# Performance work log

Measured on AMD Instinct MI355X. Metric: run time of the kernel, lower is better.

The kernel has to match this reference:

```python
import jax, jax.numpy as jnp
import numpy as np

EPS = 1e-12   # F.normalize eps
COS_EPS = 1e-8  # F.cosine_similarity eps

B, S, V, D, P, L = 4, 2048, 64, 1024, 8, 24
H = D // 24            # prefix_transform bottleneck = 42
K = 2 * L * D          # 49152 output feature dim


def setup_inputs() -> dict:
    key = jax.random.key(0)
    ks = jax.random.split(key, 8)
    return {
        "prefix": jax.random.randint(ks[0], (B, V), 0, V),
        "ctx_embeds": jax.random.normal(ks[1], (B, S, D), jnp.float32),
        "tables": jax.random.normal(ks[2], (P, V, D), jnp.float32) * 0.02,
        "lora_prefix_emb": jax.random.normal(ks[3], (P, D), jnp.float32),
        "w1": jax.random.normal(ks[4], (D, H), jnp.float32) * 0.02,
        "b1": jnp.zeros((H,), jnp.float32),
        "w2": jax.random.normal(ks[5], (H, K), jnp.float32) * 0.02,
        "b2": jnp.zeros((K,), jnp.float32),
    }


def _gates(ctx_embeds, lora_prefix_emb):
    """select_prefix, vectorized over the num_prefix_set loop.

    The original builds sim_i = bmm(norm(emb), norm(e_i.repeat(B,S,1), dim=0).permute)
    of shape [B,S,S]; since the key is repeated, every column of sim is identical,
    so we carry the column vector [P,B,S] and the math is exact.
    """
    b, s, _ = ctx_embeds.shape
    # normalize embedding over feature dim (F.normalize p=2 dim=2)
    emb_n = ctx_embeds / jnp.maximum(
        jnp.linalg.norm(ctx_embeds, axis=2, keepdims=True), EPS)
    # F.normalize over dim=0 of a tensor repeated B times -> sign(x)/sqrt(B)
    u = lora_prefix_emb / jnp.maximum(
        jnp.sqrt(float(b)) * jnp.abs(lora_prefix_emb), EPS)  # [P,D]
    v = jnp.einsum('bsd,pd->pbs', emb_n, u)          # column of sim matrix
    c = jnp.maximum(v, 0.0)                          # clamp(min=0)
    # F.normalize over last dim (length S, all entries equal c) -> c/(sqrt(S)*c)
    n = c / jnp.maximum(jnp.sqrt(float(s)) * c, EPS)
    w = jax.nn.softmax(n, axis=2)                    # softmax over token dim (dim=1 in torch layout)
    a_v = jnp.einsum('pbs,bsd->pbd', w, ctx_embeds)  # attended value per expert
    e_norm = jnp.linalg.norm(lora_prefix_emb, axis=1)          # [P]
    a_norm = jnp.linalg.norm(a_v, axis=2)                      # [P,B]
    cos = jnp.einsum('pd,pbd->pb', lora_prefix_emb, a_v) / \
        jnp.maximum(e_norm[:, None] * a_norm, COS_EPS)
    return jax.nn.softmax(cos.T, axis=-1)            # self.s_t, [B,P]


def reference(prefix, ctx_embeds, tables, lora_prefix_emb, w1, b1, w2, b2):
    s_t = _gates(ctx_embeds, lora_prefix_emb)        # [B,P]
    # forward() re-applies softmax to self.s_t (faithful double softmax)
    gate = jax.nn.softmax(s_t, axis=-1)              # [B,P]
    tok = tables[:, prefix]                          # [P,B,V,D] per-expert embedding lookup
    h = jnp.tanh(jnp.einsum('pbvd,dh->pbvh', tok, w1) + b1)
    pkv = jnp.einsum('pbvh,hk->pbvk', h, w2) + b2    # [P,B,V,K]
    out = jnp.einsum('bp,pbvk->bvk', gate, pkv)      # gated mixture over experts
    return out
```

## Files before the change

kernel.cpp:

```cpp
#include <hip/hip_runtime.h>

#define BB 4
#define SS 2048
#define VV 64
#define DD 1024
#define PP 8
#define HH 42
#define KK 49152

static constexpr float F_EPS = 1e-12f;
static constexpr float SQRT_S = 45.254833995939045f;

__global__ __launch_bounds__(256) void k1_rowdots(
    const float* __restrict__ ctx, const float* __restrict__ lora,
    float* __restrict__ n_ws) {
  __shared__ float u_lds[PP * DD];
  const int t = threadIdx.x;
  for (int i = t; i < PP * DD; i += 256) {
    float e = lora[i];
    u_lds[i] = e / fmaxf(2.0f * fabsf(e), F_EPS);
  }
  __syncthreads();
  const int wave = t >> 6, lane = t & 63;
  const float4* ctx4 = (const float4*)ctx;
  const float4* u4 = (const float4*)u_lds;
  #pragma unroll
  for (int i = 0; i < 4; ++i) {
    const int r = blockIdx.x * 16 + wave * 4 + i;
    float sumsq = 0.0f;
    float dot[PP];
    #pragma unroll
    for (int p = 0; p < PP; ++p) dot[p] = 0.0f;
    #pragma unroll
    for (int j = 0; j < 4; ++j) {
      float4 c = ctx4[(size_t)r * 256 + j * 64 + lane];
      sumsq += c.x * c.x + c.y * c.y + c.z * c.z + c.w * c.w;
      #pragma unroll
      for (int p = 0; p < PP; ++p) {
        float4 u = u4[p * 256 + j * 64 + lane];
        dot[p] += c.x * u.x + c.y * u.y + c.z * u.z + c.w * u.w;
      }
    }
    #pragma unroll
    for (int m = 32; m >= 1; m >>= 1) {
      sumsq += __shfl_xor(sumsq, m, 64);
      #pragma unroll
      for (int p = 0; p < PP; ++p) dot[p] += __shfl_xor(dot[p], m, 64);
    }
    if (lane == 0) {
      float inv = 1.0f / fmaxf(sqrtf(sumsq), F_EPS);
      float nn[PP];
      #pragma unroll
      for (int p = 0; p < PP; ++p) {
        float v = dot[p] * inv;
        float c = fmaxf(v, 0.0f);
        nn[p] = c / fmaxf(SQRT_S * c, F_EPS);
      }
      float4* o = (float4*)(n_ws + (size_t)r * 8);
      o[0] = make_float4(nn[0], nn[1], nn[2], nn[3]);
      o[1] = make_float4(nn[4], nn[5], nn[6], nn[7]);
    }
  }
}

__global__ __launch_bounds__(256) void k3_av(
    const float* __restrict__ ctx, const float* __restrict__ n_ws,
    float* __restrict__ part) {
  const int t = threadIdx.x;
  const int chunk = blockIdx.x;
  const int b = blockIdx.y;
  const int dz = blockIdx.z;
  __shared__ float zpart[4][PP];
  __shared__ float Zl[PP];
  __shared__ float w_lds[64 * PP];
  float z[PP];
  #pragma unroll
  for (int p = 0; p < PP; ++p) z[p] = 0.0f;
  const float4* n4 = (const float4*)n_ws;
  for (int it = 0; it < 8; ++it) {
    int s = it * 256 + t;
    float4 a = n4[(size_t)(b * SS + s) * 2];
    float4 c = n4[(size_t)(b * SS + s) * 2 + 1];
    z[0] += expf(a.x); z[1] += expf(a.y); z[2] += expf(a.z); z[3] += expf(a.w);
    z[4] += expf(c.x); z[5] += expf(c.y); z[6] += expf(c.z); z[7] += expf(c.w);
  }
  #pragma unroll
  for (int m = 32; m >= 1; m >>= 1) {
    #pragma unroll
    for (int p = 0; p < PP; ++p) z[p] += __shfl_xor(z[p], m, 64);
  }
  const int wave = t >> 6, lane = t & 63;
  if (lane == 0) {
    #pragma unroll
    for (int p = 0; p < PP; ++p) zpart[wave][p] = z[p];
  }
  __syncthreads();
  if (t < PP) Zl[t] = zpart[0][t] + zpart[1][t] + zpart[2][t] + zpart[3][t];
  __syncthreads();
  if (t < 64) {
    int s = chunk * 64 + t;
    #pragma unroll
    for (int p = 0; p < PP; ++p)
      w_lds[t * PP + p] = expf(n_ws[(size_t)(b * SS + s) * 8 + p]) / Zl[p];
  }
  __syncthreads();
  float2 acc[PP];
  #pragma unroll
  for (int p = 0; p < PP; ++p) acc[p] = make_float2(0.f, 0.f);
  const float2* ctx2 = (const float2*)ctx;
  const float4* w4 = (const float4*)w_lds;
  #pragma unroll 4
  for (int sl = 0; sl < 64; ++sl) {
    int s = chunk * 64 + sl;
    float2 c = ctx2[(size_t)(b * SS + s) * 512 + dz * 256 + t];
    float4 wa = w4[sl * 2];
    float4 wb = w4[sl * 2 + 1];
    float w[PP] = {wa.x, wa.y, wa.z, wa.w, wb.x, wb.y, wb.z, wb.w};
    #pragma unroll
    for (int p = 0; p < PP; ++p) {
      acc[p].x += w[p] * c.x;
      acc[p].y += w[p] * c.y;
    }
  }
  float2* part2 = (float2*)part;
  #pragma unroll
  for (int p = 0; p < PP; ++p)
    part2[(size_t)((b * 32 + chunk) * PP + p) * 512 + dz * 256 + t] = acc[p];
}

__global__ __launch_bounds__(256) void k4_cos(
    const float* __restrict__ part, const float* __restrict__ lora,
    float* __restrict__ cos_ws) {
  const int t = threadIdx.x;
  const int p = blockIdx.x, b = blockIdx.y;
  const float4* part4 = (const float4*)part;
  float4 av = make_float4(0.f, 0.f, 0.f, 0.f);
  for (int c = 0; c < 32; ++c) {
    float4 x = part4[(size_t)((b * 32 + c) * PP + p) * 256 + t];
    av.x += x.x; av.y += x.y; av.z += x.z; av.w += x.w;
  }
  float4 e = ((const float4*)lora)[p * 256 + t];
  float dt = av.x * e.x + av.y * e.y + av.z * e.z + av.w * e.w;
  float a2 = av.x * av.x + av.y * av.y + av.z * av.z + av.w * av.w;
  float e2 = e.x * e.x + e.y * e.y + e.z * e.z + e.w * e.w;
  #pragma unroll
  for (int m = 32; m >= 1; m >>= 1) {
    dt += __shfl_xor(dt, m, 64);
    a2 += __shfl_xor(a2, m, 64);
    e2 += __shfl_xor(e2, m, 64);
  }
  __shared__ float red[4][3];
  const int wave = t >> 6, lane = t & 63;
  if (lane == 0) { red[wave][0] = dt; red[wave][1] = a2; red[wave][2] = e2; }
  __syncthreads();
  if (t == 0) {
    float Dv = red[0][0] + red[1][0] + red[2][0] + red[3][0];
    float Av = red[0][1] + red[1][1] + red[2][1] + red[3][1];
    float Ev = red[0][2] + red[1][2] + red[2][2] + red[3][2];
    cos_ws[b * PP + p] = Dv / fmaxf(sqrtf(Ev) * sqrtf(Av), 1e-8f);
  }
}

__global__ __launch_bounds__(256) void k5_hall(
    const float* __restrict__ tables, const float* __restrict__ w1,
    const float* __restrict__ b1, float* __restrict__ h_all) {
  __shared__ float row_lds[DD];
  __shared__ float partial[4 * 64];
  const int t = threadIdx.x;
  const int r = blockIdx.x;
  ((float4*)row_lds)[t] = ((const float4*)(tables + (size_t)r * DD))[t];
  __syncthreads();
  const int h = t & 63, q = t >> 6;
  float acc = 0.0f;
  if (h < HH) {
    const int d0 = q * 256;
    #pragma unroll 8
    for (int dl = 0; dl < 256; ++dl) {
      acc += row_lds[d0 + dl] * w1[(size_t)(d0 + dl) * HH + h];
    }
  }
  partial[q * 64 + h] = acc;
  __syncthreads();
  if (t < HH) {
    float s = partial[t] + partial[64 + t] + partial[128 + t] + partial[192 + t];
    h_all[(size_t)r * HH + t] = tanhf(s + b1[t]);
  }
}

__global__ __launch_bounds__(256) void k7_out(
    const float* __restrict__ w2, const float* __restrict__ b2,
    const float* __restrict__ h_all, const float* __restrict__ cos_ws,
    const int* __restrict__ prefix, float* __restrict__ out) {
  __shared__ float gate_lds[PP];
  __shared__ float hg_lds[HH * 64];
  __shared__ float w2_lds[HH * 128];
  const int t = threadIdx.x;
  const int b = blockIdx.y;
  const size_t kbase = (size_t)blockIdx.x * 128;
  for (int i = t; i < HH * 128; i += 256) {
    int h = i >> 7, kk = i & 127;
    w2_lds[i] = w2[(size_t)h * KK + kbase + kk];
  }
  if (t == 0) {
    float c[PP];
    float m = -1e30f;
    #pragma unroll
    for (int p = 0; p < PP; ++p) { c[p] = cos_ws[b * PP + p]; m = fmaxf(m, c[p]); }
    float s = 0.0f;
    #pragma unroll
    for (int p = 0; p < PP; ++p) { c[p] = expf(c[p] - m); s += c[p]; }
    float inv = 1.0f / s;
    float m2 = -1e30f;
    #pragma unroll
    for (int p = 0; p < PP; ++p) { c[p] *= inv; m2 = fmaxf(m2, c[p]); }
    float s2 = 0.0f;
    #pragma unroll
    for (int p = 0; p < PP; ++p) { c[p] = expf(c[p] - m2); s2 += c[p]; }
    float inv2 = 1.0f / s2;
    #pragma unroll
    for (int p = 0; p < PP; ++p) gate_lds[p] = c[p] * inv2;
  }
  __syncthreads();
  for (int idx = t; idx < 64 * HH; idx += 256) {
    int v = idx / HH;
    int h = idx - v * HH;
    int tokv = prefix[b * VV + v];
    float s = 0.0f;
    #pragma unroll
    for (int p = 0; p < PP; ++p)
      s += gate_lds[p] * h_all[(size_t)(p * VV + tokv) * HH + h];
    hg_lds[h * 64 + v] = s;
  }
  __syncthreads();
  const int tk = t & 31, tb = t >> 5;
  float4 acc[8];
  #pragma unroll
  for (int i = 0; i < 8; ++i) acc[i] = make_float4(0.f, 0.f, 0.f, 0.f);
  const float4* w24 = (const float4*)w2_lds;
  const float4* hg4 = (const float4*)hg_lds;
  #pragma unroll 2
  for (int h = 0; h < HH; ++h) {
    float4 wv = w24[h * 32 + tk];
    float4 g0 = hg4[h * 16 + tb * 2];
    float4 g1 = hg4[h * 16 + tb * 2 + 1];
    float gg[8] = {g0.x, g0.y, g0.z, g0.w, g1.x, g1.y, g1.z, g1.w};
    #pragma unroll
    for (int i = 0; i < 8; ++i) {
      acc[i].x += gg[i] * wv.x;
      acc[i].y += gg[i] * wv.y;
      acc[i].z += gg[i] * wv.z;
      acc[i].w += gg[i] * wv.w;
    }
  }
  float4 b2v = ((const float4*)b2)[(kbase >> 2) + tk];
  float4* out4 = (float4*)out;
  #pragma unroll
  for (int i = 0; i < 8; ++i) {
    int bv = b * 64 + tb * 8 + i;
    float4 o;
    o.x = acc[i].x + b2v.x;
    o.y = acc[i].y + b2v.y;
    o.z = acc[i].z + b2v.z;
    o.w = acc[i].w + b2v.w;
    out4[(((size_t)bv * KK + kbase) >> 2) + tk] = o;
  }
}

extern "C" void kernel_launch(void* const* d_in, const int* in_sizes, int n_in,
                              void* d_out, int out_size, void* d_ws, size_t ws_size,
                              hipStream_t stream) {
  const int* prefix = (const int*)d_in[0];
  const float* ctx = (const float*)d_in[1];
  const float* tables = (const float*)d_in[2];
  const float* lora = (const float*)d_in[3];
  const float* w1 = (const float*)d_in[4];
  const float* b1 = (const float*)d_in[5];
  const float* w2 = (const float*)d_in[6];
  const float* b2 = (const float*)d_in[7];
  float* out = (float*)d_out;
  char* ws = (char*)d_ws;
  float* n_ws = (float*)ws;
  float* part = (float*)(ws + 262144);
  float* cos_ws = (float*)(ws + 262144 + 4194304);
  float* h_all = (float*)(ws + 262144 + 4194304 + 128);

  k1_rowdots<<<512, 256, 0, stream>>>(ctx, lora, n_ws);
  k5_hall<<<512, 256, 0, stream>>>(tables, w1, b1, h_all);
  k3_av<<<dim3(32, 4, 2), 256, 0, stream>>>(ctx, n_ws, part);
  k4_cos<<<dim3(8, 4), 256, 0, stream>>>(part, lora, cos_ws);
  k7_out<<<dim3(384, 4), 256, 0, stream>>>(w2, b2, h_all, cos_ws, prefix, out);
}
```

Before: 170.0 us.

## Fuse row-dot and hidden-projection kernels into one launch with batched rows

Merges the ctx row-dot gating kernel and the tables×w1 hidden projection into one 1024-block launch, with block index choosing the branch, so the two independent stages run concurrently and one launch is saved. The row-dot branch now loads four rows at once to reuse each LDS u vector and raise memory-level parallelism. It also replaces the per-expert full butterfly with a partial reduce plus a select-and-transpose shuffle, so eight lanes write results. The fused kernel allocates 32KB of LDS for every block, including the small hidden-projection blocks, which may reduce their occupancy. A partial-sum loop in k4_cos also gets an unroll pragma.

```diff
diff --git a/kernel.cpp b/kernel.cpp
--- a/kernel.cpp
+++ b/kernel.cpp
@@ -11,54 +11,95 @@
 static constexpr float F_EPS = 1e-12f;
 static constexpr float SQRT_S = 45.254833995939045f;
 
-__global__ __launch_bounds__(256) void k1_rowdots(
+__global__ __launch_bounds__(256) void k15_fused(
     const float* __restrict__ ctx, const float* __restrict__ lora,
-    float* __restrict__ n_ws) {
-  __shared__ float u_lds[PP * DD];
+    const float* __restrict__ tables, const float* __restrict__ w1,
+    const float* __restrict__ b1, float* __restrict__ n_ws,
+    float* __restrict__ h_all) {
+  __shared__ float smem[PP * DD];
   const int t = threadIdx.x;
-  for (int i = t; i < PP * DD; i += 256) {
-    float e = lora[i];
-    u_lds[i] = e / fmaxf(2.0f * fabsf(e), F_EPS);
-  }
-  __syncthreads();
-  const int wave = t >> 6, lane = t & 63;
-  const float4* ctx4 = (const float4*)ctx;
-  const float4* u4 = (const float4*)u_lds;
-  #pragma unroll
-  for (int i = 0; i < 4; ++i) {
-    const int r = blockIdx.x * 16 + wave * 4 + i;
-    float sumsq = 0.0f;
-    float dot[PP];
-    #pragma unroll
-    for (int p = 0; p < PP; ++p) dot[p] = 0.0f;
+  if (blockIdx.x < 512) {
+    for (int i = t; i < PP * DD; i += 256) {
+      float e = lora[i];
+      smem[i] = e / fmaxf(2.0f * fabsf(e), F_EPS);
+    }
+    __syncthreads();
+    const int wave = t >> 6, lane = t & 63;
+    const int rbase = blockIdx.x * 16 + wave * 4;
+    const float4* ctx4 = (const float4*)ctx;
+    const float4* u4 = (const float4*)smem;
+    float dot[4][PP];
+    float sq[4] = {0.f, 0.f, 0.f, 0.f};
+    #pragma unroll
+    for (int i = 0; i < 4; ++i)
+      #pragma unroll
+      for (int p = 0; p < PP; ++p) dot[i][p] = 0.f;
     #pragma unroll
     for (int j = 0; j < 4; ++j) {
-      float4 c = ctx4[(size_t)r * 256 + j * 64 + lane];
-      sumsq += c.x * c.x + c.y * c.y + c.z * c.z + c.w * c.w;
+      float4 c[4];
+      #pragma unroll
+      for (int i = 0; i < 4; ++i)
+        c[i] = ctx4[(size_t)(rbase + i) * 256 + j * 64 + lane];
+      #pragma unroll
+      for (int i = 0; i < 4; ++i)
+        sq[i] += c[i].x * c[i].x + c[i].y * c[i].y + c[i].z * c[i].z + c[i].w * c[i].w;
       #pragma unroll
       for (int p = 0; p < PP; ++p) {
         float4 u = u4[p * 256 + j * 64 + lane];
-        dot[p] += c.x * u.x + c.y * u.y + c.z * u.z + c.w * u.w;
+        #pragma unroll
+        for (int i = 0; i < 4; ++i)
+          dot[i][p] += c[i].x * u.x + c[i].y * u.y + c[i].z * u.z + c[i].w * u.w;
       }
     }
-    #pragma unroll
-    for (int m = 32; m >= 1; m >>= 1) {
-      sumsq += __shfl_xor(sumsq, m, 64);
-      #pragma unroll
-      for (int p = 0; p < PP; ++p) dot[p] += __shfl_xor(dot[p], m, 64);
-    }
-    if (lane == 0) {
-      float inv = 1.0f / fmaxf(sqrtf(sumsq), F_EPS);
-      float nn[PP];
-      #pragma unroll
-      for (int p = 0; p < PP; ++p) {
-        float v = dot[p] * inv;
-        float c = fmaxf(v, 0.0f);
-        nn[p] = c / fmaxf(SQRT_S * c, F_EPS);
+    const int sel = lane & 7;
+    #pragma unroll
+    for (int i = 0; i < 4; ++i) {
+      float s = sq[i];
+      #pragma unroll
+      for (int m = 32; m >= 1; m >>= 1) s += __shfl_xor(s, m, 64);
+      float d0 = dot[i][0], d1 = dot[i][1], d2 = dot[i][2], d3 = dot[i][3];
+      float d4 = dot[i][4], d5 = dot[i][5], d6 = dot[i][6], d7 = dot[i][7];
+      #pragma unroll
+      for (int m = 1; m <= 4; m <<= 1) {
+        d0 += __shfl_xor(d0, m, 64); d1 += __shfl_xor(d1, m, 64);
+        d2 += __shfl_xor(d2, m, 64); d3 += __shfl_xor(d3, m, 64);
+        d4 += __shfl_xor(d4, m, 64); d5 += __shfl_xor(d5, m, 64);
+        d6 += __shfl_xor(d6, m, 64); d7 += __shfl_xor(d7, m, 64);
       }
-      float4* o = (float4*)(n_ws + (size_t)r * 8);
-      o[0] = make_float4(nn[0], nn[1], nn[2], nn[3]);
-      o[1] = make_float4(nn[4], nn[5], nn[6], nn[7]);
+      float v = d0;
+      v = (sel == 1) ? d1 : v; v = (sel == 2) ? d2 : v;
+      v = (sel == 3) ? d3 : v; v = (sel == 4) ? d4 : v;
+      v = (sel == 5) ? d5 : v; v = (sel == 6) ? d6 : v;
+      v = (sel == 7) ? d7 : v;
+      v += __shfl_xor(v, 8, 64);
+      v += __shfl_xor(v, 16, 64);
+      v += __shfl_xor(v, 32, 64);
+      if (lane < PP) {
+        float inv = 1.0f / fmaxf(sqrtf(s), F_EPS);
+        float c = fmaxf(v * inv, 0.0f);
+        n_ws[(size_t)(rbase + i) * 8 + lane] = c / fmaxf(SQRT_S * c, F_EPS);
+      }
+    }
+  } else {
+    float* row_lds = smem;
+    float* partial = smem + DD;
+    const int r = blockIdx.x - 512;
+    ((float4*)row_lds)[t] = ((const float4*)(tables + (size_t)r * DD))[t];
+    __syncthreads();
+    const int h = t & 63, q = t >> 6;
+    float acc = 0.0f;
+    if (h < HH) {
+      const int d0 = q * 256;
+      #pragma unroll 8
+      for (int dl = 0; dl < 256; ++dl) {
+        acc += row_lds[d0 + dl] * w1[(size_t)(d0 + dl) * HH + h];
+      }
+    }
+    partial[q * 64 + h] = acc;
+    __syncthreads();
+    if (t < HH) {
+      float s = partial[t] + partial[64 + t] + partial[128 + t] + partial[192 + t];
+      h_all[(size_t)r * HH + t] = tanhf(s + b1[t]);
     }
   }
 }
@@ -135,6 +176,7 @@
   const int p = blockIdx.x, b = blockIdx.y;
   const float4* part4 = (const float4*)part;
   float4 av = make_float4(0.f, 0.f, 0.f, 0.f);
+  #pragma unroll 8
   for (int c = 0; c < 32; ++c) {
     float4 x = part4[(size_t)((b * 32 + c) * PP + p) * 256 + t];
     av.x += x.x; av.y += x.y; av.z += x.z; av.w += x.w;
@@ -158,32 +200,6 @@
     float Av = red[0][1] + red[1][1] + red[2][1] + red[3][1];
     float Ev = red[0][2] + red[1][2] + red[2][2] + red[3][2];
     cos_ws[b * PP + p] = Dv / fmaxf(sqrtf(Ev) * sqrtf(Av), 1e-8f);
-  }
-}
-
-__global__ __launch_bounds__(256) void k5_hall(
-    const float* __restrict__ tables, const float* __restrict__ w1,
-    const float* __restrict__ b1, float* __restrict__ h_all) {
-  __shared__ float row_lds[DD];
-  __shared__ float partial[4 * 64];
-  const int t = threadIdx.x;
-  const int r = blockIdx.x;
-  ((float4*)row_lds)[t] = ((const float4*)(tables + (size_t)r * DD))[t];
-  __syncthreads();
-  const int h = t & 63, q = t >> 6;
-  float acc = 0.0f;
-  if (h < HH) {
-    const int d0 = q * 256;
-    #pragma unroll 8
-    for (int dl = 0; dl < 256; ++dl) {
-      acc += row_lds[d0 + dl] * w1[(size_t)(d0 + dl) * HH + h];
-    }
-  }
-  partial[q * 64 + h] = acc;
-  __syncthreads();
-  if (t < HH) {
-    float s = partial[t] + partial[64 + t] + partial[128 + t] + partial[192 + t];
-    h_all[(size_t)r * HH + t] = tanhf(s + b1[t]);
   }
 }
 
@@ -284,8 +300,7 @@
   float* cos_ws = (float*)(ws + 262144 + 4194304);
   float* h_all = (float*)(ws + 262144 + 4194304 + 128);
 
-  k1_rowdots<<<512, 256, 0, stream>>>(ctx, lora, n_ws);
-  k5_hall<<<512, 256, 0, stream>>>(tables, w1, b1, h_all);
+  k15_fused<<<1024, 256, 0, stream>>>(ctx, lora, tables, w1, b1, n_ws, h_all);
   k3_av<<<dim3(32, 4, 2), 256, 0, stream>>>(ctx, n_ws, part);
   k4_cos<<<dim3(8, 4), 256, 0, stream>>>(part, lora, cos_ws);
   k7_out<<<dim3(384, 4), 256, 0, stream>>>(w2, b2, h_all, cos_ws, prefix, out);
```

After: 161.9 us. 4.8% less time.
